# Performance work log

Hardware: AMD Instinct MI355X
Metric: run time of the kernel (lower is better)

Reference implementation:

```python
import jax, jax.numpy as jnp
import numpy as np

B, S, D, F, E, TOP_K = 2, 2048, 1024, 2048, 8, 2


def setup_inputs() -> dict:
    key = jax.random.key(0)
    k0, k1, k2, k3 = jax.random.split(key, 4)
    return {
        "hidden_states": jax.random.normal(k0, (B, S, D), jnp.float32),
        "gate_w": jax.random.normal(k1, (E, D), jnp.float32) * 0.02,   # torch Linear weight [out=E, in=D]
        "w1": jax.random.normal(k2, (E, D, F), jnp.float32) * 0.02,    # per-expert up-proj
        "w2": jax.random.normal(k3, (E, F, D), jnp.float32) * 0.02,    # per-expert down-proj
    }


def reference(hidden_states, gate_w, w1, w2):
    b, s, d = hidden_states.shape
    e = gate_w.shape[0]
    x = hidden_states.reshape(-1, d)                 # [T, D]
    t = x.shape[0]
    router_logits = x @ gate_w.T                     # [T, E]
    # softmax in fp32 as in original, then renormalized top-k weights
    probs = jax.nn.softmax(router_logits.astype(jnp.float32), axis=-1)
    topw, sel = jax.lax.top_k(probs, TOP_K)          # [T, K]
    topw = topw / jnp.sum(topw, axis=-1, keepdims=True)
    topw = topw.astype(x.dtype)
    # dense combine weights: zero for unselected experts (top_k indices are distinct)
    combine = jnp.zeros((t, e), x.dtype).at[jnp.arange(t)[:, None], sel].add(topw)  # [T, E]
    out = jnp.zeros_like(x)
    for ei in range(e):  # small fixed expert count
        h = jax.nn.silu(x @ w1[ei]) @ w2[ei]         # [T, D]
        out = out + combine[:, ei:ei + 1] * h
    return out.reshape(b, s, d), router_logits
```

## Files before the change

kernel.cpp:

```cpp
#include <hip/hip_runtime.h>
#include <hip/hip_bf16.h>
#include <math.h>

#define Tt 4096
#define Dd 1024
#define Ff 2048
#define Ee 8

typedef unsigned short u16;
typedef short bf16x8 __attribute__((ext_vector_type(8)));
typedef float f32x4 __attribute__((ext_vector_type(4)));

__device__ __forceinline__ u16 f2bf(float f) {
  union { float f; unsigned u; } v; v.f = f;
  unsigned r = v.u + 0x7fffu + ((v.u >> 16) & 1u);
  return (u16)(r >> 16);
}

__device__ __forceinline__ void gload16(const void* g, void* l) {
  __builtin_amdgcn_global_load_lds(
      (const __attribute__((address_space(1))) unsigned int*)g,
      (__attribute__((address_space(3))) unsigned int*)l, 16, 0, 0);
}

__global__ __launch_bounds__(256) void router_kernel(
    const float* __restrict__ x, const float* __restrict__ gw,
    float* __restrict__ logits)
{
  int t = blockIdx.x * 4 + (threadIdx.x >> 6);
  int lane = threadIdx.x & 63;
  const float* xr = x + (size_t)t * Dd;
  float xv[16];
#pragma unroll
  for (int i = 0; i < 4; ++i) {
    float4 v = *reinterpret_cast<const float4*>(xr + lane * 16 + i * 4);
    xv[i*4+0] = v.x; xv[i*4+1] = v.y; xv[i*4+2] = v.z; xv[i*4+3] = v.w;
  }
#pragma unroll
  for (int e = 0; e < Ee; ++e) {
    const float* gr = gw + (size_t)e * Dd + lane * 16;
    float s = 0.f;
#pragma unroll
    for (int i = 0; i < 4; ++i) {
      float4 g = *reinterpret_cast<const float4*>(gr + i * 4);
      s += xv[i*4+0]*g.x + xv[i*4+1]*g.y + xv[i*4+2]*g.z + xv[i*4+3]*g.w;
    }
#pragma unroll
    for (int o = 32; o > 0; o >>= 1) s += __shfl_xor(s, o);
    if (lane == 0) logits[(size_t)t * Ee + e] = s;
  }
}

__global__ __launch_bounds__(256) void build_kernel(
    const float* __restrict__ logits, int* __restrict__ meta,
    int* __restrict__ list, float* __restrict__ wgt)
{
  __shared__ int hist[16], cur[16];
  const int tid = threadIdx.x;
  const int lane = tid & 63;
  if (tid < 16) hist[tid] = 0;
  __syncthreads();
  for (int it = 0; it < Tt / 256; ++it) {
    int t = it * 256 + tid;
    float4 lo = *reinterpret_cast<const float4*>(logits + (size_t)t * 8);
    float4 hi = *reinterpret_cast<const float4*>(logits + (size_t)t * 8 + 4);
    float s[8] = {lo.x, lo.y, lo.z, lo.w, hi.x, hi.y, hi.z, hi.w};
    int i1 = 0; float m1 = s[0];
#pragma unroll
    for (int e = 1; e < 8; ++e) if (s[e] > m1) { m1 = s[e]; i1 = e; }
    int i2 = -1; float m2 = -__builtin_inff();
#pragma unroll
    for (int e = 0; e < 8; ++e) if (e != i1 && s[e] > m2) { m2 = s[e]; i2 = e; }
#pragma unroll
    for (int k = 0; k < 2; ++k) {
      int gg = k ? (8 + i2) : i1;
      unsigned long long m = ~0ull;
#pragma unroll
      for (int b = 0; b < 4; ++b) {
        unsigned long long vb = __ballot((gg >> b) & 1);
        m &= ((gg >> b) & 1) ? vb : ~vb;
      }
      int rank = __popcll(m & ((1ull << lane) - 1));
      if (rank == 0) atomicAdd(&hist[gg], __popcll(m));
    }
  }
  __syncthreads();
  if (tid == 0) {
    int sacc = 0;
    for (int g = 0; g < 16; ++g) {
      meta[g] = hist[g];
      meta[32 + g] = sacc;
      cur[g] = sacc;
      sacc += hist[g];
    }
  }
  __syncthreads();
  for (int it = 0; it < Tt / 256; ++it) {
    int t = it * 256 + tid;
    float4 lo = *reinterpret_cast<const float4*>(logits + (size_t)t * 8);
    float4 hi = *reinterpret_cast<const float4*>(logits + (size_t)t * 8 + 4);
    float s[8] = {lo.x, lo.y, lo.z, lo.w, hi.x, hi.y, hi.z, hi.w};
    int i1 = 0; float m1 = s[0];
#pragma unroll
    for (int e = 1; e < 8; ++e) if (s[e] > m1) { m1 = s[e]; i1 = e; }
    int i2 = -1; float m2 = -__builtin_inff();
#pragma unroll
    for (int e = 0; e < 8; ++e) if (e != i1 && s[e] > m2) { m2 = s[e]; i2 = e; }
    float wa = 1.f / (1.f + expf(m2 - m1));
#pragma unroll
    for (int k = 0; k < 2; ++k) {
      int gg = k ? (8 + i2) : i1;
      float w = k ? (1.f - wa) : wa;
      unsigned long long m = ~0ull;
#pragma unroll
      for (int b = 0; b < 4; ++b) {
        unsigned long long vb = __ballot((gg >> b) & 1);
        m &= ((gg >> b) & 1) ? vb : ~vb;
      }
      int rank = __popcll(m & ((1ull << lane) - 1));
      int ldr = __ffsll(m) - 1;
      int base = 0;
      if (rank == 0) base = atomicAdd(&cur[gg], __popcll(m));
      base = __shfl(base, ldr);
      list[base + rank] = t;
      wgt[base + rank] = w;
    }
  }
}

__global__ __launch_bounds__(256) void cvt_bf16_kernel(
    const float* __restrict__ in, u16* __restrict__ out, int n4)
{
  int i = blockIdx.x * 256 + threadIdx.x;
  if (i >= n4) return;
  float4 v = reinterpret_cast<const float4*>(in)[i];
  ushort4 b;
  b.x = f2bf(v.x); b.y = f2bf(v.y); b.z = f2bf(v.z); b.w = f2bf(v.w);
  reinterpret_cast<ushort4*>(out)[i] = b;
}

__global__ __launch_bounds__(256) void transpose_bf16_kernel(
    const float* __restrict__ in, u16* __restrict__ out, int R, int C)
{
  __shared__ u16 st[64][65];
  const size_t eoff = (size_t)blockIdx.z * R * C;
  const float* ip = in + eoff;
  u16* op = out + eoff;
  int r0 = blockIdx.y * 64, c0 = blockIdx.x * 64;
  int t = threadIdx.x;
  int rr = t >> 2;
  int cb = (t & 3) * 16;
#pragma unroll
  for (int i = 0; i < 4; ++i) {
    float4 v = *reinterpret_cast<const float4*>(ip + (size_t)(r0 + rr) * C + c0 + cb + i * 4);
    st[rr][cb + i*4 + 0] = f2bf(v.x);
    st[rr][cb + i*4 + 1] = f2bf(v.y);
    st[rr][cb + i*4 + 2] = f2bf(v.z);
    st[rr][cb + i*4 + 3] = f2bf(v.w);
  }
  __syncthreads();
#pragma unroll
  for (int i = 0; i < 4; ++i) {
    ushort4 b;
    b.x = st[cb + i*4 + 0][rr];
    b.y = st[cb + i*4 + 1][rr];
    b.z = st[cb + i*4 + 2][rr];
    b.w = st[cb + i*4 + 3][rr];
    *reinterpret_cast<ushort4*>(op + (size_t)(c0 + rr) * R + r0 + cb + i * 4) = b;
  }
}

template<int BM, int MODE, int N_, int K_>
__global__ __launch_bounds__(256) void gemm_g(
    const u16* __restrict__ Abase, const u16* __restrict__ Bbase,
    void* __restrict__ Cout, const int* __restrict__ meta,
    const int* __restrict__ list, const float* __restrict__ wgt)
{
  constexpr int BN  = 128;
  constexpr int WGR = BM / 64;
  constexpr int WGC = 4 / WGR;
  constexpr int WN  = BN / WGC;
  constexpr int NFR = WN / 16;
  constexpr int CA  = BM / 64;
  constexpr int ABUF = BM * 32;
  constexpr int BBUF = BN * 32;

  __shared__ u16 Al[2 * ABUF];
  __shared__ u16 Bl[2 * BBUF];

  const int g   = blockIdx.z;
  const int e   = g & 7;
  const int cnt = meta[g];
  const int rb  = blockIdx.y;
  if (rb * BM >= cnt) return;
  const int off = meta[32 + g];

  const int tid  = threadIdx.x;
  const int lane = tid & 63;
  const int wave = tid >> 6;
  const int wr   = (WGR == 2) ? (wave >> 1) : 0;
  const int wc   = (WGR == 2) ? (wave & 1) : wave;
  const int n0   = blockIdx.x * BN;

  const int l4 = lane >> 2;
  const int kc = (lane & 3) * 8;

  const u16* aptr[CA];
  u16* alds[CA];
#pragma unroll
  for (int c = 0; c < CA; ++c) {
    int chunk = wave * CA + c;
    int row = chunk * 16 + l4;
    int i = rb * BM + row;
    if (i >= cnt) i = cnt - 1;
    int srow = (MODE == 0) ? list[off + i] : (off + i);
    aptr[c] = Abase + (size_t)srow * K_ + kc;
    alds[c] = Al + chunk * 512;
  }
  const u16* bptr[2];
  u16* blds[2];
#pragma unroll
  for (int c = 0; c < 2; ++c) {
    int chunk = wave * 2 + c;
    int row = chunk * 16 + l4;
    bptr[c] = Bbase + ((size_t)e * N_ + n0 + row) * K_ + kc;
    blds[c] = Bl + chunk * 512;
  }

  f32x4 acc[4][NFR] = {};
  const int r16 = lane & 15;
  const int kq  = (lane >> 4) * 8;
  constexpr int NT = K_ / 32;

#pragma unroll
  for (int c = 0; c < CA; ++c) gload16(aptr[c], alds[c]);
#pragma unroll
  for (int c = 0; c < 2; ++c) gload16(bptr[c], blds[c]);
  __syncthreads();

  int cur = 0;
  for (int t = 0; t < NT; ++t) {
    if (t + 1 < NT) {
      int k0 = (t + 1) * 32;
      int nb = cur ^ 1;
#pragma unroll
      for (int c = 0; c < CA; ++c) gload16(aptr[c] + k0, alds[c] + nb * ABUF);
#pragma unroll
      for (int c = 0; c < 2; ++c) gload16(bptr[c] + k0, blds[c] + nb * BBUF);
    }
    const u16* Ab = Al + cur * ABUF;
    const u16* Bb = Bl + cur * BBUF;
    bf16x8 af[4], bfv[NFR];
#pragma unroll
    for (int m = 0; m < 4; ++m)
      af[m] = *reinterpret_cast<const bf16x8*>(&Ab[(wr*64 + m*16 + r16) * 32 + kq]);
#pragma unroll
    for (int n = 0; n < NFR; ++n)
      bfv[n] = *reinterpret_cast<const bf16x8*>(&Bb[(wc*WN + n*16 + r16) * 32 + kq]);
#pragma unroll
    for (int m = 0; m < 4; ++m)
#pragma unroll
      for (int n = 0; n < NFR; ++n)
        acc[m][n] = __builtin_amdgcn_mfma_f32_16x16x32_bf16(af[m], bfv[n], acc[m][n], 0, 0, 0);
    __syncthreads();
    cur ^= 1;
  }

  const int colb = n0 + wc * WN + r16;
  const int rb4  = wr * 64 + ((lane >> 4) << 2);
#pragma unroll
  for (int m = 0; m < 4; ++m) {
#pragma unroll
    for (int r = 0; r < 4; ++r) {
      int i = rb * BM + rb4 + m * 16 + r;
      if (i >= cnt) continue;
      if (MODE == 0) {
        u16* hp = (u16*)Cout + (size_t)(off + i) * N_;
#pragma unroll
        for (int n = 0; n < NFR; ++n) {
          float v = acc[m][n][r];
          v = v / (1.f + expf(-v));
          hp[colb + n * 16] = f2bf(v);
        }
      } else {
        int   tok = list[off + i];
        float w   = wgt[off + i];
        float* o = (float*)Cout + (size_t)tok * N_;
#pragma unroll
        for (int n = 0; n < NFR; ++n)
          atomicAdd(&o[colb + n * 16], w * acc[m][n][r]);
      }
    }
  }
}

__global__ __launch_bounds__(256) void combine_kernel(
    const float* __restrict__ logits, float* __restrict__ combine)
{
  int t = blockIdx.x * 256 + threadIdx.x;
  if (t >= Tt) return;
  float4 lo = *reinterpret_cast<const float4*>(logits + (size_t)t * 8);
  float4 hi = *reinterpret_cast<const float4*>(logits + (size_t)t * 8 + 4);
  float s[8] = {lo.x, lo.y, lo.z, lo.w, hi.x, hi.y, hi.z, hi.w};
  int i1 = 0; float m1 = s[0];
#pragma unroll
  for (int e = 1; e < 8; ++e) if (s[e] > m1) { m1 = s[e]; i1 = e; }
  int i2 = -1; float m2 = -__builtin_inff();
#pragma unroll
  for (int e = 0; e < 8; ++e) if (e != i1 && s[e] > m2) { m2 = s[e]; i2 = e; }
  float wa = 1.f / (1.f + expf(m2 - m1));
#pragma unroll
  for (int e = 0; e < 8; ++e)
    combine[(size_t)t * 8 + e] = (e == i1) ? wa : ((e == i2) ? (1.f - wa) : 0.f);
}

template<int MODE, int N_, int K_>
__global__ __launch_bounds__(256) void gemm_dense(
    const float* __restrict__ A, const float* __restrict__ Bg,
    float* __restrict__ C, const float* __restrict__ combine,
    int expert, int first)
{
  constexpr int BM = 128, BN = 128, BK = 32, LDT = 40;
  __shared__ u16 Al[BM * LDT];
  __shared__ u16 Bl[BN * LDT];
  const int tid  = threadIdx.x;
  const int lane = tid & 63;
  const int wave = tid >> 6;
  const int wr = wave >> 1, wc = wave & 1;
  const int m0 = blockIdx.y * BM;
  const int n0 = blockIdx.x * BN;
  f32x4 acc[4][4] = {};
  for (int k0 = 0; k0 < K_; k0 += BK) {
#pragma unroll
    for (int i = 0; i < 4; ++i) {
      int f = tid + 256 * i;
      int row = f >> 3;
      int c4 = (f & 7) << 2;
      float4 v = *reinterpret_cast<const float4*>(A + (size_t)(m0 + row) * K_ + k0 + c4);
      ushort4 b;
      b.x = f2bf(v.x); b.y = f2bf(v.y); b.z = f2bf(v.z); b.w = f2bf(v.w);
      *reinterpret_cast<ushort4*>(&Al[row * LDT + c4]) = b;
    }
    {
      int n  = tid & 127;
      int kb = (tid >> 7) << 4;
      const float* bp = Bg + (size_t)(k0 + kb) * N_ + n0 + n;
      u16 tmp[16];
#pragma unroll
      for (int kk = 0; kk < 16; ++kk)
        tmp[kk] = f2bf(bp[(size_t)kk * N_]);
      u16* p = &Bl[n * LDT + kb];
#pragma unroll
      for (int i = 0; i < 4; ++i) {
        ushort4 b;
        b.x = tmp[i*4+0]; b.y = tmp[i*4+1]; b.z = tmp[i*4+2]; b.w = tmp[i*4+3];
        *reinterpret_cast<ushort4*>(p + i * 4) = b;
      }
    }
    __syncthreads();
    bf16x8 af[4], bfr[4];
    const int kq  = (lane >> 4) << 3;
    const int r16 = lane & 15;
#pragma unroll
    for (int m = 0; m < 4; ++m)
      af[m] = *reinterpret_cast<const bf16x8*>(&Al[(wr*64 + m*16 + r16) * LDT + kq]);
#pragma unroll
    for (int n = 0; n < 4; ++n)
      bfr[n] = *reinterpret_cast<const bf16x8*>(&Bl[(wc*64 + n*16 + r16) * LDT + kq]);
#pragma unroll
    for (int m = 0; m < 4; ++m)
#pragma unroll
      for (int n = 0; n < 4; ++n)
        acc[m][n] = __builtin_amdgcn_mfma_f32_16x16x32_bf16(af[m], bfr[n], acc[m][n], 0, 0, 0);
    __syncthreads();
  }
  const int col0 = n0 + wc * 64 + (lane & 15);
  const int rbs  = m0 + wr * 64 + ((lane >> 4) << 2);
#pragma unroll
  for (int m = 0; m < 4; ++m) {
#pragma unroll
    for (int r = 0; r < 4; ++r) {
      int row = rbs + m * 16 + r;
      if (MODE == 0) {
#pragma unroll
        for (int n = 0; n < 4; ++n) {
          float v = acc[m][n][r];
          v = v / (1.f + expf(-v));
          C[(size_t)row * N_ + col0 + n * 16] = v;
        }
      } else {
        float w = combine[(size_t)row * Ee + expert];
        if (first) {
#pragma unroll
          for (int n = 0; n < 4; ++n)
            C[(size_t)row * N_ + col0 + n * 16] = w * acc[m][n][r];
        } else {
#pragma unroll
          for (int n = 0; n < 4; ++n)
            C[(size_t)row * N_ + col0 + n * 16] += w * acc[m][n][r];
        }
      }
    }
  }
}

extern "C" void kernel_launch(void* const* d_in, const int* in_sizes, int n_in,
                              void* d_out, int out_size, void* d_ws, size_t ws_size,
                              hipStream_t stream)
{
  const float* x  = (const float*)d_in[0];
  const float* gw = (const float*)d_in[1];
  const float* w1 = (const float*)d_in[2];
  const float* w2 = (const float*)d_in[3];
  float* out    = (float*)d_out;
  float* logits = out + (size_t)Tt * Dd;

  int*   meta = (int*)d_ws;
  int*   list = (int*)((char*)d_ws + 256);
  float* wgt  = (float*)((char*)d_ws + 256 + 32768);
  u16*   xb   = (u16*)((char*)d_ws + 262144);
  u16*   h1   = (u16*)((char*)d_ws + 262144 + 8388608);
  u16*   wT   = (u16*)((char*)d_ws + 262144 + 8388608 + 33554432);
  const size_t NEED = 262144ull + 8388608ull + 33554432ull + 33554432ull;

  router_kernel<<<Tt / 4, 256, 0, stream>>>(x, gw, logits);

  if (ws_size >= NEED) {
    hipMemsetAsync(out, 0, (size_t)Tt * Dd * sizeof(float), stream);
    build_kernel<<<1, 256, 0, stream>>>(logits, meta, list, wgt);
    cvt_bf16_kernel<<<(Tt * Dd / 4) / 256, 256, 0, stream>>>(x, xb, Tt * Dd / 4);
    transpose_bf16_kernel<<<dim3(Ff/64, Dd/64, Ee), 256, 0, stream>>>(w1, wT, Dd, Ff);
    gemm_g<128, 0, Ff, Dd><<<dim3(Ff/128, 32, 16), 256, 0, stream>>>(xb, wT, h1, meta, list, wgt);
    transpose_bf16_kernel<<<dim3(Dd/64, Ff/64, Ee), 256, 0, stream>>>(w2, wT, Ff, Dd);
    gemm_g<64, 1, Dd, Ff><<<dim3(Dd/128, 64, 16), 256, 0, stream>>>(h1, wT, out, meta, list, wgt);
  } else {
    float* combine = (float*)d_ws;
    float* h1d     = combine + (size_t)Tt * Ee;
    combine_kernel<<<Tt / 256, 256, 0, stream>>>(logits, combine);
    size_t cb = (size_t)Tt * Ee * sizeof(float);
    size_t avail = ws_size > cb ? (ws_size - cb) : 0;
    long maxrows = (long)(avail / ((size_t)Ff * sizeof(float)));
    int chunk = (maxrows >= Tt) ? Tt : (int)((maxrows / 128) * 128);
    if (chunk < 128) chunk = 128;
    for (int c0 = 0; c0 < Tt; c0 += chunk) {
      int rows = (Tt - c0) < chunk ? (Tt - c0) : chunk;
      for (int e = 0; e < Ee; ++e) {
        gemm_dense<0, Ff, Dd><<<dim3(Ff/128, rows/128), 256, 0, stream>>>(
            x + (size_t)c0 * Dd, w1 + (size_t)e * Dd * Ff, h1d, nullptr, e, 0);
        gemm_dense<1, Dd, Ff><<<dim3(Dd/128, rows/128), 256, 0, stream>>>(
            h1d, w2 + (size_t)e * Ff * Dd, out + (size_t)c0 * Dd,
            combine + (size_t)c0 * Ee, e, (e == 0) ? 1 : 0);
      }
    }
  }
}
```

Before: 235.8 us.

## Merge top-1/top-2 expert groups and swizzle grouped GEMM blocks across XCDs

```diff
diff --git a/kernel.cpp b/kernel.cpp
--- a/kernel.cpp
+++ b/kernel.cpp
@@ -55,10 +55,10 @@
     const float* __restrict__ logits, int* __restrict__ meta,
     int* __restrict__ list, float* __restrict__ wgt)
 {
-  __shared__ int hist[16], cur[16];
+  __shared__ int hist[8], cur[8];
   const int tid = threadIdx.x;
   const int lane = tid & 63;
-  if (tid < 16) hist[tid] = 0;
+  if (tid < 8) hist[tid] = 0;
   __syncthreads();
   for (int it = 0; it < Tt / 256; ++it) {
     int t = it * 256 + tid;
@@ -73,10 +73,10 @@
     for (int e = 0; e < 8; ++e) if (e != i1 && s[e] > m2) { m2 = s[e]; i2 = e; }
 #pragma unroll
     for (int k = 0; k < 2; ++k) {
-      int gg = k ? (8 + i2) : i1;
+      int gg = k ? i2 : i1;
       unsigned long long m = ~0ull;
 #pragma unroll
-      for (int b = 0; b < 4; ++b) {
+      for (int b = 0; b < 3; ++b) {
         unsigned long long vb = __ballot((gg >> b) & 1);
         m &= ((gg >> b) & 1) ? vb : ~vb;
       }
@@ -87,7 +87,7 @@
   __syncthreads();
   if (tid == 0) {
     int sacc = 0;
-    for (int g = 0; g < 16; ++g) {
+    for (int g = 0; g < 8; ++g) {
       meta[g] = hist[g];
       meta[32 + g] = sacc;
       cur[g] = sacc;
@@ -109,11 +109,11 @@
     float wa = 1.f / (1.f + expf(m2 - m1));
 #pragma unroll
     for (int k = 0; k < 2; ++k) {
-      int gg = k ? (8 + i2) : i1;
+      int gg = k ? i2 : i1;
       float w = k ? (1.f - wa) : wa;
       unsigned long long m = ~0ull;
 #pragma unroll
-      for (int b = 0; b < 4; ++b) {
+      for (int b = 0; b < 3; ++b) {
         unsigned long long vb = __ballot((gg >> b) & 1);
         m &= ((gg >> b) & 1) ? vb : ~vb;
       }
@@ -170,48 +170,50 @@
   }
 }
 
-template<int BM, int MODE, int N_, int K_>
+template<int MODE, int N_, int K_>
 __global__ __launch_bounds__(256) void gemm_g(
     const u16* __restrict__ Abase, const u16* __restrict__ Bbase,
     void* __restrict__ Cout, const int* __restrict__ meta,
     const int* __restrict__ list, const float* __restrict__ wgt)
 {
-  constexpr int BN  = 128;
-  constexpr int WGR = BM / 64;
-  constexpr int WGC = 4 / WGR;
-  constexpr int WN  = BN / WGC;
-  constexpr int NFR = WN / 16;
-  constexpr int CA  = BM / 64;
-  constexpr int ABUF = BM * 32;
-  constexpr int BBUF = BN * 32;
+  constexpr int BM = 128, BN = 128;
+  constexpr int NXc = N_ / BN;
+  constexpr int NYc = 32;
+  constexpr int NWG = NXc * NYc * 8;
+  constexpr int CPX = NWG / 8;
+  constexpr int ABUF = BM * 32, BBUF = BN * 32;
 
   __shared__ u16 Al[2 * ABUF];
   __shared__ u16 Bl[2 * BBUF];
 
-  const int g   = blockIdx.z;
-  const int e   = g & 7;
-  const int cnt = meta[g];
-  const int rb  = blockIdx.y;
-  if (rb * BM >= cnt) return;
-  const int off = meta[32 + g];
+  const int orig = blockIdx.x + NXc * (blockIdx.y + NYc * blockIdx.z);
+  const int swz  = (orig & 7) * CPX + (orig >> 3);
+  const int bz   = swz / (NXc * NYc);
+  const int rem  = swz - bz * (NXc * NYc);
+  const int by   = rem / NXc;
+  const int bx   = rem - by * NXc;
+
+  const int e   = bz;
+  const int cnt = meta[e];
+  if (by * BM >= cnt) return;
+  const int off = meta[32 + e];
 
   const int tid  = threadIdx.x;
   const int lane = tid & 63;
   const int wave = tid >> 6;
-  const int wr   = (WGR == 2) ? (wave >> 1) : 0;
-  const int wc   = (WGR == 2) ? (wave & 1) : wave;
-  const int n0   = blockIdx.x * BN;
+  const int wr   = wave >> 1, wc = wave & 1;
+  const int n0   = bx * BN;
 
   const int l4 = lane >> 2;
   const int kc = (lane & 3) * 8;
 
-  const u16* aptr[CA];
-  u16* alds[CA];
-#pragma unroll
-  for (int c = 0; c < CA; ++c) {
-    int chunk = wave * CA + c;
+  const u16* aptr[2];
+  u16* alds[2];
+#pragma unroll
+  for (int c = 0; c < 2; ++c) {
+    int chunk = wave * 2 + c;
     int row = chunk * 16 + l4;
-    int i = rb * BM + row;
+    int i = by * BM + row;
     if (i >= cnt) i = cnt - 1;
     int srow = (MODE == 0) ? list[off + i] : (off + i);
     aptr[c] = Abase + (size_t)srow * K_ + kc;
@@ -227,13 +229,13 @@
     blds[c] = Bl + chunk * 512;
   }
 
-  f32x4 acc[4][NFR] = {};
+  f32x4 acc[4][4] = {};
   const int r16 = lane & 15;
   const int kq  = (lane >> 4) * 8;
   constexpr int NT = K_ / 32;
 
 #pragma unroll
-  for (int c = 0; c < CA; ++c) gload16(aptr[c], alds[c]);
+  for (int c = 0; c < 2; ++c) gload16(aptr[c], alds[c]);
 #pragma unroll
   for (int c = 0; c < 2; ++c) gload16(bptr[c], blds[c]);
   __syncthreads();
@@ -244,40 +246,40 @@
       int k0 = (t + 1) * 32;
       int nb = cur ^ 1;
 #pragma unroll
-      for (int c = 0; c < CA; ++c) gload16(aptr[c] + k0, alds[c] + nb * ABUF);
+      for (int c = 0; c < 2; ++c) gload16(aptr[c] + k0, alds[c] + nb * ABUF);
 #pragma unroll
       for (int c = 0; c < 2; ++c) gload16(bptr[c] + k0, blds[c] + nb * BBUF);
     }
     const u16* Ab = Al + cur * ABUF;
     const u16* Bb = Bl + cur * BBUF;
-    bf16x8 af[4], bfv[NFR];
+    bf16x8 af[4], bfv[4];
 #pragma unroll
     for (int m = 0; m < 4; ++m)
       af[m] = *reinterpret_cast<const bf16x8*>(&Ab[(wr*64 + m*16 + r16) * 32 + kq]);
 #pragma unroll
-    for (int n = 0; n < NFR; ++n)
-      bfv[n] = *reinterpret_cast<const bf16x8*>(&Bb[(wc*WN + n*16 + r16) * 32 + kq]);
+    for (int n = 0; n < 4; ++n)
+      bfv[n] = *reinterpret_cast<const bf16x8*>(&Bb[(wc*64 + n*16 + r16) * 32 + kq]);
 #pragma unroll
     for (int m = 0; m < 4; ++m)
 #pragma unroll
-      for (int n = 0; n < NFR; ++n)
+      for (int n = 0; n < 4; ++n)
         acc[m][n] = __builtin_amdgcn_mfma_f32_16x16x32_bf16(af[m], bfv[n], acc[m][n], 0, 0, 0);
     __syncthreads();
     cur ^= 1;
   }
 
-  const int colb = n0 + wc * WN + r16;
+  const int colb = n0 + wc * 64 + r16;
   const int rb4  = wr * 64 + ((lane >> 4) << 2);
 #pragma unroll
   for (int m = 0; m < 4; ++m) {
 #pragma unroll
     for (int r = 0; r < 4; ++r) {
-      int i = rb * BM + rb4 + m * 16 + r;
+      int i = by * BM + rb4 + m * 16 + r;
       if (i >= cnt) continue;
       if (MODE == 0) {
         u16* hp = (u16*)Cout + (size_t)(off + i) * N_;
 #pragma unroll
-        for (int n = 0; n < NFR; ++n) {
+        for (int n = 0; n < 4; ++n) {
           float v = acc[m][n][r];
           v = v / (1.f + expf(-v));
           hp[colb + n * 16] = f2bf(v);
@@ -287,7 +289,7 @@
         float w   = wgt[off + i];
         float* o = (float*)Cout + (size_t)tok * N_;
 #pragma unroll
-        for (int n = 0; n < NFR; ++n)
+        for (int n = 0; n < 4; ++n)
           atomicAdd(&o[colb + n * 16], w * acc[m][n][r]);
       }
     }
@@ -430,9 +432,9 @@
     build_kernel<<<1, 256, 0, stream>>>(logits, meta, list, wgt);
     cvt_bf16_kernel<<<(Tt * Dd / 4) / 256, 256, 0, stream>>>(x, xb, Tt * Dd / 4);
     transpose_bf16_kernel<<<dim3(Ff/64, Dd/64, Ee), 256, 0, stream>>>(w1, wT, Dd, Ff);
-    gemm_g<128, 0, Ff, Dd><<<dim3(Ff/128, 32, 16), 256, 0, stream>>>(xb, wT, h1, meta, list, wgt);
+    gemm_g<0, Ff, Dd><<<dim3(Ff/128, 32, 8), 256, 0, stream>>>(xb, wT, h1, meta, list, wgt);
     transpose_bf16_kernel<<<dim3(Dd/64, Ff/64, Ee), 256, 0, stream>>>(w2, wT, Ff, Dd);
-    gemm_g<64, 1, Dd, Ff><<<dim3(Dd/128, 64, 16), 256, 0, stream>>>(h1, wT, out, meta, list, wgt);
+    gemm_g<1, Dd, Ff><<<dim3(Dd/128, 32, 8), 256, 0, stream>>>(h1, wT, out, meta, list, wgt);
   } else {
     float* combine = (float*)d_ws;
     float* h1d     = combine + (size_t)Tt * Ee;
```

New measurement: 217.8 us. 1.08x faster.
